# Optimization experiments

Hardware: AMD Instinct MI355X
Metric: run time of the kernel (lower is better)

Reference implementation:

```python
import jax, jax.numpy as jnp
import numpy as np

FACTOR = 5

def setup_inputs() -> dict:
    key = jax.random.key(0)
    k1, k2, k3 = jax.random.split(key, 3)
    B, L, H, D = 4, 2048, 8, 64
    logL = int(np.ceil(np.log(L)))          # 8
    U_part = min(2 * FACTOR * logL, L)      # 80 sampled keys per query
    queries = jax.random.normal(k1, (B, L, H, D), dtype=jnp.float32)
    keys = jax.random.normal(k2, (B, L, H, D), dtype=jnp.float32)
    index_sample = jax.random.randint(k3, (L, U_part), 0, L)
    return {"queries": queries, "keys": keys, "index_sample": index_sample}

def reference(queries, keys, index_sample):
    B, L, H, D = queries.shape
    q = jnp.transpose(queries, (0, 2, 1, 3))   # [B,H,L,D]
    k = jnp.transpose(keys, (0, 2, 1, 3))      # [B,H,L,D]
    logL = int(np.ceil(np.log(L)))
    u = min(FACTOR * logL, L)                  # n_top queries

    # sample keys per query position: [B,H,L,S,D]
    K_sample = k[:, :, index_sample, :]
    # Q_i . K_sample_ij : [B,H,L,S]
    QK_sample = jnp.einsum('bhld,bhlsd->bhls', q, K_sample)
    # sparsity measure M = max - mean (mean over full L as in source)
    M = QK_sample.max(axis=-1) - QK_sample.sum(axis=-1) / L   # [B,H,L]
    _, M_top = jax.lax.top_k(M, u)                            # [B,H,u]

    # gather selected queries and compute full scores against all keys
    Q_reduce = jnp.take_along_axis(q, M_top[..., None], axis=2)  # [B,H,u,D]
    scale = 1.0 / jnp.sqrt(jnp.float32(D))
    scores = jnp.einsum('bhud,bhld->bhul', Q_reduce, k) * scale  # [B,H,u,L]
    attn = jax.nn.softmax(scores, axis=-1)

    # scatter softmaxed rows into full [B,H,L,L] attention matrix (rest zeros)
    out = jnp.zeros((B, H, L, L), dtype=attn.dtype)
    b_idx = jnp.arange(B)[:, None, None]
    h_idx = jnp.arange(H)[None, :, None]
    out = out.at[b_idx, h_idx, M_top, :].set(attn)
    return out
```

## Files before the change

### kernel.cpp

```cpp
#include <hip/hip_runtime.h>
#include <math.h>

#define NB 4
#define NL 2048
#define NH 8
#define ND 64
#define NUPART 80
#define NUTOP 40

__global__ __launch_bounds__(256) void k_compute_M(
    const float* __restrict__ q, const float* __restrict__ k,
    const int* __restrict__ idx, float* __restrict__ M)
{
    const int w    = blockIdx.x * 4 + (threadIdx.x >> 6);
    const int lane = threadIdx.x & 63;
    const int l    = w & (NL - 1);
    const int bh   = w >> 11;
    const int h    = bh & (NH - 1);
    const int b    = bh >> 3;
    const int sl   = lane >> 2;
    const int dg   = lane & 3;
    const int d0   = dg * 16;

    const float4* qv = (const float4*)(q + (((size_t)(b * NL + l) * NH + h) * ND + d0));
    const float4 q0 = qv[0], q1 = qv[1], q2 = qv[2], q3 = qv[3];

    float mx = -INFINITY, sm = 0.0f;
#pragma unroll
    for (int r = 0; r < 5; ++r) {
        const int s  = r * 16 + sl;
        const int ki = idx[l * NUPART + s];
        const float4* kv = (const float4*)(k + (((size_t)(b * NL + ki) * NH + h) * ND + d0));
        const float4 k0 = kv[0], k1 = kv[1], k2 = kv[2], k3 = kv[3];
        float p = q0.x * k0.x + q0.y * k0.y + q0.z * k0.z + q0.w * k0.w
                + q1.x * k1.x + q1.y * k1.y + q1.z * k1.z + q1.w * k1.w
                + q2.x * k2.x + q2.y * k2.y + q2.z * k2.z + q2.w * k2.w
                + q3.x * k3.x + q3.y * k3.y + q3.z * k3.z + q3.w * k3.w;
        p += __shfl_xor(p, 1);
        p += __shfl_xor(p, 2);
        mx = fmaxf(mx, p);
        sm += p;
    }
#pragma unroll
    for (int m = 4; m < 64; m <<= 1) {
        mx = fmaxf(mx, __shfl_xor(mx, m));
        sm += __shfl_xor(sm, m);
    }
    if (lane == 0) M[w] = mx - sm * (1.0f / (float)NL);
}

__global__ __launch_bounds__(256) void k_topk(
    const float* __restrict__ M, int* __restrict__ Mtop)
{
    __shared__ float sM[NL];
    __shared__ float rv[4];
    __shared__ int   ri[4];
    const int bh = blockIdx.x;
    const int t  = threadIdx.x;

    for (int j = t; j < NL; j += 256) sM[j] = M[bh * NL + j];
    __syncthreads();

    for (int it = 0; it < NUTOP; ++it) {
        float v = -INFINITY;
        int   i = NL;
        for (int j = t; j < NL; j += 256) {
            const float m = sM[j];
            if (m > v || (m == v && j < i)) { v = m; i = j; }
        }
#pragma unroll
        for (int off = 1; off < 64; off <<= 1) {
            const float ov = __shfl_xor(v, off);
            const int   oi = __shfl_xor(i, off);
            if (ov > v || (ov == v && oi < i)) { v = ov; i = oi; }
        }
        const int wid = t >> 6;
        if ((t & 63) == 0) { rv[wid] = v; ri[wid] = i; }
        __syncthreads();
        if (t == 0) {
            for (int w2 = 1; w2 < 4; ++w2) {
                if (rv[w2] > v || (rv[w2] == v && ri[w2] < i)) { v = rv[w2]; i = ri[w2]; }
            }
            Mtop[bh * NUTOP + it] = i;
            sM[i] = -INFINITY;
        }
        __syncthreads();
    }
}

__global__ __launch_bounds__(256) void k_attn(
    const float* __restrict__ q, const float* __restrict__ k,
    const int* __restrict__ Mtop, float* __restrict__ out)
{
    __shared__ float redm[4];
    __shared__ float reds[4];

    const int bh  = blockIdx.x / NUTOP;
    const int ui  = blockIdx.x % NUTOP;
    const int b   = bh >> 3;
    const int h   = bh & 7;
    const int row = Mtop[bh * NUTOP + ui];
    const int t   = threadIdx.x;
    const int lane = t & 63;
    const int wid  = t >> 6;

    const float4* qv = (const float4*)(q + (((size_t)(b * NL + row)) * NH + h) * ND);
    float4 qr[16];
#pragma unroll
    for (int i = 0; i < 16; ++i) qr[i] = qv[i];

    float sc[8];
    float mx = -INFINITY;
#pragma unroll
    for (int j = 0; j < 8; ++j) {
        const int l = t + 256 * j;
        const float4* kv = (const float4*)(k + (((size_t)(b * NL + l)) * NH + h) * ND);
        float s = 0.0f;
#pragma unroll
        for (int i = 0; i < 16; ++i) {
            const float4 kk = kv[i];
            s += qr[i].x * kk.x + qr[i].y * kk.y + qr[i].z * kk.z + qr[i].w * kk.w;
        }
        sc[j] = s * 0.125f;
        mx = fmaxf(mx, sc[j]);
    }

#pragma unroll
    for (int off = 1; off < 64; off <<= 1) mx = fmaxf(mx, __shfl_xor(mx, off));
    if (lane == 0) redm[wid] = mx;
    __syncthreads();
    mx = fmaxf(fmaxf(redm[0], redm[1]), fmaxf(redm[2], redm[3]));

    float lsum = 0.0f;
#pragma unroll
    for (int j = 0; j < 8; ++j) {
        sc[j] = __expf(sc[j] - mx);
        lsum += sc[j];
    }
#pragma unroll
    for (int off = 1; off < 64; off <<= 1) lsum += __shfl_xor(lsum, off);
    if (lane == 0) reds[wid] = lsum;
    __syncthreads();
    const float inv = 1.0f / (reds[0] + reds[1] + reds[2] + reds[3]);

    float* orow = out + ((size_t)bh * NL + row) * NL;
#pragma unroll
    for (int j = 0; j < 8; ++j) {
        orow[t + 256 * j] = sc[j] * inv;
    }
}

extern "C" void kernel_launch(void* const* d_in, const int* in_sizes, int n_in,
                              void* d_out, int out_size, void* d_ws, size_t ws_size,
                              hipStream_t stream) {
    const float* q   = (const float*)d_in[0];
    const float* k   = (const float*)d_in[1];
    const int*   idx = (const int*)d_in[2];
    float* out = (float*)d_out;

    float* Mws  = (float*)d_ws;
    int*   Mtop = (int*)((char*)d_ws + (size_t)NB * NH * NL * 4);

    hipMemsetAsync(out, 0, (size_t)out_size * sizeof(float), stream);

    k_compute_M<<<NB * NH * NL / 4, 256, 0, stream>>>(q, k, idx, Mws);
    k_topk<<<NB * NH, 256, 0, stream>>>(Mws, Mtop);
    k_attn<<<NB * NH * NUTOP, 256, 0, stream>>>(q, k, Mtop, out);
}
```

Baseline: 408.9 us.

## Fuse output zero-fill into per-row attention kernel with nontemporal stores

Drops the separate memset of the full BxHxLxL output. The top-k kernel now writes a per-row selection flag map instead of an index list. A new kernel launches one block per output row: unselected rows are zero-filled with vector nontemporal stores, and selected rows compute the softmax row directly. This removes the double write of the selected rows and lets the large zero-fill use streaming stores instead of the runtime memset. The cost is a much larger workspace for the row map and many tiny blocks.

```diff
diff --git a/kernel.cpp b/kernel.cpp
--- a/kernel.cpp
+++ b/kernel.cpp
@@ -7,6 +7,8 @@
 #define ND 64
 #define NUPART 80
 #define NUTOP 40
+
+typedef float vfloat4 __attribute__((ext_vector_type(4)));
 
 __global__ __launch_bounds__(256) void k_compute_M(
     const float* __restrict__ q, const float* __restrict__ k,
@@ -50,7 +52,7 @@
 }
 
 __global__ __launch_bounds__(256) void k_topk(
-    const float* __restrict__ M, int* __restrict__ Mtop)
+    const float* __restrict__ M, int* __restrict__ rowmap)
 {
     __shared__ float sM[NL];
     __shared__ float rv[4];
@@ -58,7 +60,10 @@
     const int bh = blockIdx.x;
     const int t  = threadIdx.x;
 
-    for (int j = t; j < NL; j += 256) sM[j] = M[bh * NL + j];
+    for (int j = t; j < NL; j += 256) {
+        sM[j] = M[bh * NL + j];
+        rowmap[bh * NL + j] = 0;
+    }
     __syncthreads();
 
     for (int it = 0; it < NUTOP; ++it) {
@@ -81,26 +86,35 @@
             for (int w2 = 1; w2 < 4; ++w2) {
                 if (rv[w2] > v || (rv[w2] == v && ri[w2] < i)) { v = rv[w2]; i = ri[w2]; }
             }
-            Mtop[bh * NUTOP + it] = i;
+            rowmap[bh * NL + i] = 1;
             sM[i] = -INFINITY;
         }
         __syncthreads();
     }
 }
 
-__global__ __launch_bounds__(256) void k_attn(
+__global__ __launch_bounds__(256) void k_out(
     const float* __restrict__ q, const float* __restrict__ k,
-    const int* __restrict__ Mtop, float* __restrict__ out)
+    const int* __restrict__ rowmap, float* __restrict__ out)
 {
+    const int r   = blockIdx.x;
+    const int bh  = r >> 11;
+    const int row = r & (NL - 1);
+    const int b   = bh >> 3;
+    const int h   = bh & 7;
+    const int t   = threadIdx.x;
+
+    vfloat4* orow = (vfloat4*)(out + (size_t)r * NL);
+
+    if (!rowmap[r]) {
+        const vfloat4 z = (vfloat4)(0.0f);
+        __builtin_nontemporal_store(z, orow + t);
+        __builtin_nontemporal_store(z, orow + t + 256);
+        return;
+    }
+
     __shared__ float redm[4];
     __shared__ float reds[4];
-
-    const int bh  = blockIdx.x / NUTOP;
-    const int ui  = blockIdx.x % NUTOP;
-    const int b   = bh >> 3;
-    const int h   = bh & 7;
-    const int row = Mtop[bh * NUTOP + ui];
-    const int t   = threadIdx.x;
     const int lane = t & 63;
     const int wid  = t >> 6;
 
@@ -143,10 +157,9 @@
     __syncthreads();
     const float inv = 1.0f / (reds[0] + reds[1] + reds[2] + reds[3]);
 
-    float* orow = out + ((size_t)bh * NL + row) * NL;
 #pragma unroll
     for (int j = 0; j < 8; ++j) {
-        orow[t + 256 * j] = sc[j] * inv;
+        __builtin_nontemporal_store(sc[j] * inv, out + (size_t)r * NL + t + 256 * j);
     }
 }
 
@@ -158,12 +171,10 @@
     const int*   idx = (const int*)d_in[2];
     float* out = (float*)d_out;
 
-    float* Mws  = (float*)d_ws;
-    int*   Mtop = (int*)((char*)d_ws + (size_t)NB * NH * NL * 4);
-
-    hipMemsetAsync(out, 0, (size_t)out_size * sizeof(float), stream);
+    float* Mws    = (float*)d_ws;
+    int*   rowmap = (int*)((char*)d_ws + (size_t)NB * NH * NL * 4);
 
     k_compute_M<<<NB * NH * NL / 4, 256, 0, stream>>>(q, k, idx, Mws);
-    k_topk<<<NB * NH, 256, 0, stream>>>(Mws, Mtop);
-    k_attn<<<NB * NH * NUTOP, 256, 0, stream>>>(q, k, Mtop, out);
+    k_topk<<<NB * NH, 256, 0, stream>>>(Mws, rowmap);
+    k_out<<<NB * NH * NL, 256, 0, stream>>>(q, k, rowmap, out);
 }
```

Result: no change. 413.0 us (+1.0%).
